# Kernel tuning notes

Hardware: AMD Instinct MI355X
Metric: run time of the kernel (lower is better)

The kernel has to match this reference:

```python
import jax, jax.numpy as jnp
import numpy as np

VOCAB = 50257
EMBED_DIM = 1024
FRONT_DIM = 2048  # int(embed_dim * front_embed_mul)
BATCH, SEQ = 4, 4096


def setup_inputs() -> dict:
    key = jax.random.key(0)
    k_idx, k_emb, k_w1, k_b1, k_w2, k_b2 = jax.random.split(key, 6)
    idxs = jax.random.randint(k_idx, (BATCH, SEQ), 0, VOCAB, dtype=jnp.int64)
    tok_embed = jax.random.normal(k_emb, (VOCAB, FRONT_DIM), dtype=jnp.float32)
    # torch nn.Linear weights are [out, in]
    W1 = jax.random.normal(k_w1, (EMBED_DIM, FRONT_DIM), dtype=jnp.float32) * (1.0 / np.sqrt(FRONT_DIM))
    b1 = jax.random.normal(k_b1, (EMBED_DIM,), dtype=jnp.float32) * 0.01
    W2 = jax.random.normal(k_w2, (EMBED_DIM, EMBED_DIM), dtype=jnp.float32) * (1.0 / np.sqrt(EMBED_DIM))
    b2 = jax.random.normal(k_b2, (EMBED_DIM,), dtype=jnp.float32) * 0.01
    return {"idxs": idxs, "tok_embed": tok_embed, "W1": W1, "b1": b1, "W2": W2, "b2": b2}


def reference(idxs, tok_embed, W1, b1, W2, b2):
    # Embedding gather: [B, S, front_dim]
    x = tok_embed[idxs]
    # integration1: Linear(front_dim -> embed_dim)
    x = jnp.einsum('bsf,ef->bse', x, W1) + b1
    # exact (erf-based) GELU, matching torch F.gelu default
    x = jax.nn.gelu(x, approximate=False)
    # integration2: Linear(embed_dim -> embed_dim)
    x = jnp.einsum('bse,oe->bso', x, W2) + b2
    return x
```

## Files before the change

kernel.cpp:

```cpp
#include <hip/hip_runtime.h>
#include <hip/hip_bf16.h>

typedef __attribute__((ext_vector_type(4))) float floatx4;
typedef __attribute__((ext_vector_type(8))) short short8;
typedef __attribute__((ext_vector_type(8))) unsigned short ushortx8;

#define K1 2048
#define N1 1024
#define K2 1024
#define N2 1024

__device__ __forceinline__ unsigned short f2bf(float f) {
  __hip_bfloat16 h = __float2bfloat16(f);
  return __builtin_bit_cast(unsigned short, h);
}

__device__ __forceinline__ void gload_lds16(const void* g, void* l) {
  __builtin_amdgcn_global_load_lds(
      (__attribute__((address_space(1))) void*)const_cast<void*>(g),
      (__attribute__((address_space(3))) void*)l, 16, 0, 0);
}

__global__ void cvt_bf16_kernel(const float* __restrict__ src,
                                unsigned short* __restrict__ dst, int n4) {
  int i = blockIdx.x * blockDim.x + threadIdx.x;
  if (i >= n4) return;
  float4 f = reinterpret_cast<const float4*>(src)[i];
  ushort4 o;
  o.x = f2bf(f.x); o.y = f2bf(f.y); o.z = f2bf(f.z); o.w = f2bf(f.w);
  reinterpret_cast<ushort4*>(dst)[i] = o;
}

__global__ __launch_bounds__(512, 2) void gemm1_fused_kernel(
    const int* __restrict__ idxs, const float* __restrict__ tok,
    const unsigned short* __restrict__ W1b, const float* __restrict__ b1,
    unsigned short* __restrict__ hout) {
  __shared__ unsigned short Asub[2][16384];
  __shared__ unsigned short Bsub[2][16384];
  const int t = threadIdx.x;
  const int p = blockIdx.x;
  const int bid = (p & 7) * 32 + (p >> 3);
  const int bm = bid >> 2, bn = bid & 3;
  const int brow0 = bm * 256, bcol0 = bn * 256;
  const int lane = t & 63, w = t >> 6;
  const int wm = w >> 2, wn = w & 3;
  const int fr = lane & 15, kg2 = lane >> 4;

  const int srow = t >> 3;
  const int cg = (t & 7) ^ (srow & 7);
  const float* aqf[4];
  const unsigned short* bq[4];
#pragma unroll
  for (int q = 0; q < 4; ++q) {
    const int ridx = idxs[brow0 + srow + 64 * q];
    aqf[q] = tok + (size_t)ridx * K1 + cg * 8;
    bq[q] = W1b + (size_t)(bcol0 + srow + 64 * q) * K1 + cg * 8;
  }
  const int t8 = t * 8;

  floatx4 acc[8][4] = {};
  constexpr int NT = K1 / 64;

  float4 av[4][2];
  auto loadA = [&](int k0) {
#pragma unroll
    for (int q = 0; q < 4; ++q) {
      av[q][0] = *reinterpret_cast<const float4*>(aqf[q] + k0);
      av[q][1] = *reinterpret_cast<const float4*>(aqf[q] + k0 + 4);
    }
  };
  auto writeA = [&](int d) {
#pragma unroll
    for (int q = 0; q < 4; ++q) {
      ushortx8 u;
      u[0] = f2bf(av[q][0].x); u[1] = f2bf(av[q][0].y);
      u[2] = f2bf(av[q][0].z); u[3] = f2bf(av[q][0].w);
      u[4] = f2bf(av[q][1].x); u[5] = f2bf(av[q][1].y);
      u[6] = f2bf(av[q][1].z); u[7] = f2bf(av[q][1].w);
      *reinterpret_cast<ushortx8*>(&Asub[d][t8 + q * 4096]) = u;
    }
  };
  auto issueB = [&](int d, int k0) {
#pragma unroll
    for (int q = 0; q < 4; ++q)
      gload_lds16(bq[q] + k0, &Bsub[d][t8 + q * 4096]);
  };
  auto computeKS = [&](int cur, int ks) {
    const int sl = ((ks * 4 + kg2) ^ (fr & 7)) * 8;
    short8 bf[4];
#pragma unroll
    for (int j = 0; j < 4; ++j)
      bf[j] = *(const short8*)&Bsub[cur][(wn * 64 + j * 16 + fr) * 64 + sl];
    __builtin_amdgcn_s_setprio(1);
#pragma unroll
    for (int i = 0; i < 8; ++i) {
      const short8 af = *(const short8*)&Asub[cur][(wm * 128 + i * 16 + fr) * 64 + sl];
#pragma unroll
      for (int j = 0; j < 4; ++j)
        acc[i][j] = __builtin_amdgcn_mfma_f32_16x16x32_bf16(af, bf[j], acc[i][j], 0, 0, 0);
    }
    __builtin_amdgcn_s_setprio(0);
  };

  loadA(0);
  issueB(0, 0);
  writeA(0);
  asm volatile("s_waitcnt vmcnt(0) lgkmcnt(0)\ns_barrier" ::: "memory");

#pragma unroll 1
  for (int tt = 0; tt < NT; ++tt) {
    const int cur = tt & 1;
    const int nbuf = cur ^ 1;
    const bool pf = (tt + 1 < NT);
    const int nk = (tt + 1) * 64;
    if (pf) {
      loadA(nk);
      issueB(nbuf, nk);
    }
    computeKS(cur, 0);
    if (pf) writeA(nbuf);
    computeKS(cur, 1);
    asm volatile("s_waitcnt vmcnt(0) lgkmcnt(0)\ns_barrier" ::: "memory");
  }

  const int er0 = brow0 + wm * 128 + kg2 * 4;
  const int ec0 = bcol0 + wn * 64 + fr;
#pragma unroll
  for (int j = 0; j < 4; ++j) {
    const float bv = b1[ec0 + j * 16];
#pragma unroll
    for (int i = 0; i < 8; ++i)
#pragma unroll
      for (int r = 0; r < 4; ++r) {
        float v = acc[i][j][r] + bv;
        v = 0.5f * v * (1.0f + erff(v * 0.70710678118654752f));
        hout[(size_t)(er0 + i * 16 + r) * N1 + (ec0 + j * 16)] = f2bf(v);
      }
  }
}

__global__ __launch_bounds__(512, 2) void gemm2_kernel(
    const unsigned short* __restrict__ A, const unsigned short* __restrict__ Bw,
    const float* __restrict__ bias, float* __restrict__ out) {
  __shared__ unsigned short Asub[2][16384];
  __shared__ unsigned short Bsub[2][16384];
  const int t = threadIdx.x;
  const int p = blockIdx.x;
  const int bid = (p & 7) * 32 + (p >> 3);
  const int bm = bid >> 2, bn = bid & 3;
  const int brow0 = bm * 256, bcol0 = bn * 256;
  const int lane = t & 63, w = t >> 6;
  const int wm = w >> 2, wn = w & 3;
  const int fr = lane & 15, kg2 = lane >> 4;

  const int srow = t >> 3;
  const int cg = (t & 7) ^ (srow & 7);
  const unsigned short* aq[4];
  const unsigned short* bq[4];
#pragma unroll
  for (int q = 0; q < 4; ++q) {
    aq[q] = A + (size_t)(brow0 + srow + 64 * q) * K2 + cg * 8;
    bq[q] = Bw + (size_t)(bcol0 + srow + 64 * q) * K2 + cg * 8;
  }
  const int t8 = t * 8;

  const int arow_sh = (wm * 128 + fr) * 64;
  const int brow_sh = (wn * 64 + fr) * 64;

  floatx4 acc[8][4] = {};
  constexpr int NT = K2 / 64;

  auto stage = [&](int d, int k0) {
#pragma unroll
    for (int q = 0; q < 4; ++q) {
      gload_lds16(aq[q] + k0, &Asub[d][t8 + q * 4096]);
      gload_lds16(bq[q] + k0, &Bsub[d][t8 + q * 4096]);
    }
  };
  auto compute = [&](int cur) {
#pragma unroll
    for (int ks = 0; ks < 2; ++ks) {
      const int sl = ((ks * 4 + kg2) ^ (fr & 7)) * 8;
      short8 bf[4];
#pragma unroll
      for (int j = 0; j < 4; ++j)
        bf[j] = *reinterpret_cast<const short8*>(&Bsub[cur][brow_sh + j * 1024 + sl]);
#pragma unroll
      for (int i = 0; i < 8; ++i) {
        const short8 af = *reinterpret_cast<const short8*>(&Asub[cur][arow_sh + i * 1024 + sl]);
#pragma unroll
        for (int j = 0; j < 4; ++j)
          acc[i][j] = __builtin_amdgcn_mfma_f32_16x16x32_bf16(af, bf[j], acc[i][j], 0, 0, 0);
      }
    }
  };

  stage(0, 0);
#pragma unroll 1
  for (int it = 0; it < NT - 1; ++it) {
    const int cur = it & 1;
    stage(cur ^ 1, (it + 1) * 64);
    asm volatile("s_waitcnt vmcnt(8)\ns_barrier" ::: "memory");
    compute(cur);
    asm volatile("s_waitcnt lgkmcnt(0)\ns_barrier" ::: "memory");
  }
  asm volatile("s_waitcnt vmcnt(0)\ns_barrier" ::: "memory");
  compute((NT - 1) & 1);

  const int er0 = brow0 + wm * 128 + kg2 * 4;
  const int ec0 = bcol0 + wn * 64 + fr;
#pragma unroll
  for (int j = 0; j < 4; ++j) {
    const float bv = bias[ec0 + j * 16];
#pragma unroll
    for (int i = 0; i < 8; ++i)
#pragma unroll
      for (int r = 0; r < 4; ++r)
        out[(size_t)(er0 + i * 16 + r) * N2 + (ec0 + j * 16)] = acc[i][j][r] + bv;
  }
}

extern "C" void kernel_launch(void* const* d_in, const int* in_sizes, int n_in,
                              void* d_out, int out_size, void* d_ws, size_t ws_size,
                              hipStream_t stream) {
  const int* idxs = (const int*)d_in[0];
  const float* tok = (const float*)d_in[1];
  const float* W1 = (const float*)d_in[2];
  const float* b1 = (const float*)d_in[3];
  const float* W2 = (const float*)d_in[4];
  const float* b2 = (const float*)d_in[5];
  float* out = (float*)d_out;

  unsigned short* W1b = (unsigned short*)d_ws;
  unsigned short* W2b = (unsigned short*)((char*)d_ws + (4u << 20));
  unsigned short* hbuf = (unsigned short*)((char*)d_ws + (6u << 20));

  cvt_bf16_kernel<<<2048, 256, 0, stream>>>(W1, W1b, 524288);
  cvt_bf16_kernel<<<1024, 256, 0, stream>>>(W2, W2b, 262144);
  gemm1_fused_kernel<<<256, 512, 0, stream>>>(idxs, tok, W1b, b1, hbuf);
  gemm2_kernel<<<256, 512, 0, stream>>>(hbuf, W2b, b2, out);
}
```

Before: 155.5 us.

## Stage GEMM epilogues through LDS for coalesced stores and merge weight conversions

Both GEMM epilogues now write their accumulator tiles into a per-wave swizzled LDS region (reusing the now-unified shared buffer), then read them back as 16-byte vectors so each row segment goes to global memory as one coalesced store. Before, each lane stored scattered 2-byte or 4-byte elements. The two weight-conversion launches are merged into a single kernel to save one launch. gemm2 also gains setprio around its MFMA loop. In exchange the epilogue adds LDS traffic and waitcnt/barrier overhead.

Result: faster. 140.9 us (-9.4%).

```diff
diff --git a/kernel.cpp b/kernel.cpp
--- a/kernel.cpp
+++ b/kernel.cpp
@@ -21,22 +21,32 @@
       (__attribute__((address_space(3))) void*)l, 16, 0, 0);
 }
 
-__global__ void cvt_bf16_kernel(const float* __restrict__ src,
-                                unsigned short* __restrict__ dst, int n4) {
+__global__ __launch_bounds__(256) void cvt2_kernel(
+    const float* __restrict__ W1, const float* __restrict__ W2,
+    unsigned short* __restrict__ W1b, unsigned short* __restrict__ W2b) {
   int i = blockIdx.x * blockDim.x + threadIdx.x;
-  if (i >= n4) return;
-  float4 f = reinterpret_cast<const float4*>(src)[i];
+  const float* src;
+  unsigned short* dst;
+  if (i < 524288) {
+    src = (const float*)&reinterpret_cast<const float4*>(W1)[i];
+    dst = (unsigned short*)&reinterpret_cast<ushort4*>(W1b)[i];
+  } else {
+    int k = i - 524288;
+    if (k >= 262144) return;
+    src = (const float*)&reinterpret_cast<const float4*>(W2)[k];
+    dst = (unsigned short*)&reinterpret_cast<ushort4*>(W2b)[k];
+  }
+  float4 f = *reinterpret_cast<const float4*>(src);
   ushort4 o;
   o.x = f2bf(f.x); o.y = f2bf(f.y); o.z = f2bf(f.z); o.w = f2bf(f.w);
-  reinterpret_cast<ushort4*>(dst)[i] = o;
+  *reinterpret_cast<ushort4*>(dst) = o;
 }
 
 __global__ __launch_bounds__(512, 2) void gemm1_fused_kernel(
     const int* __restrict__ idxs, const float* __restrict__ tok,
     const unsigned short* __restrict__ W1b, const float* __restrict__ b1,
     unsigned short* __restrict__ hout) {
-  __shared__ unsigned short Asub[2][16384];
-  __shared__ unsigned short Bsub[2][16384];
+  __shared__ unsigned short S[65536];
   const int t = threadIdx.x;
   const int p = blockIdx.x;
   const int bid = (p & 7) * 32 + (p >> 3);
@@ -77,24 +87,24 @@
       u[2] = f2bf(av[q][0].z); u[3] = f2bf(av[q][0].w);
       u[4] = f2bf(av[q][1].x); u[5] = f2bf(av[q][1].y);
       u[6] = f2bf(av[q][1].z); u[7] = f2bf(av[q][1].w);
-      *reinterpret_cast<ushortx8*>(&Asub[d][t8 + q * 4096]) = u;
+      *reinterpret_cast<ushortx8*>(&S[d * 16384 + t8 + q * 4096]) = u;
     }
   };
   auto issueB = [&](int d, int k0) {
 #pragma unroll
     for (int q = 0; q < 4; ++q)
-      gload_lds16(bq[q] + k0, &Bsub[d][t8 + q * 4096]);
+      gload_lds16(bq[q] + k0, &S[32768 + d * 16384 + t8 + q * 4096]);
   };
   auto computeKS = [&](int cur, int ks) {
     const int sl = ((ks * 4 + kg2) ^ (fr & 7)) * 8;
     short8 bf[4];
 #pragma unroll
     for (int j = 0; j < 4; ++j)
-      bf[j] = *(const short8*)&Bsub[cur][(wn * 64 + j * 16 + fr) * 64 + sl];
+      bf[j] = *(const short8*)&S[32768 + cur * 16384 + (wn * 64 + j * 16 + fr) * 64 + sl];
     __builtin_amdgcn_s_setprio(1);
 #pragma unroll
     for (int i = 0; i < 8; ++i) {
-      const short8 af = *(const short8*)&Asub[cur][(wm * 128 + i * 16 + fr) * 64 + sl];
+      const short8 af = *(const short8*)&S[cur * 16384 + (wm * 128 + i * 16 + fr) * 64 + sl];
 #pragma unroll
       for (int j = 0; j < 4; ++j)
         acc[i][j] = __builtin_amdgcn_mfma_f32_16x16x32_bf16(af, bf[j], acc[i][j], 0, 0, 0);
@@ -123,27 +133,38 @@
     asm volatile("s_waitcnt vmcnt(0) lgkmcnt(0)\ns_barrier" ::: "memory");
   }
 
-  const int er0 = brow0 + wm * 128 + kg2 * 4;
   const int ec0 = bcol0 + wn * 64 + fr;
-#pragma unroll
-  for (int j = 0; j < 4; ++j) {
-    const float bv = b1[ec0 + j * 16];
-#pragma unroll
-    for (int i = 0; i < 8; ++i)
+  float bv[4];
+#pragma unroll
+  for (int j = 0; j < 4; ++j) bv[j] = b1[ec0 + j * 16];
+  unsigned short* Wl = S + w * 8192;
+#pragma unroll
+  for (int i = 0; i < 8; ++i)
+#pragma unroll
+    for (int j = 0; j < 4; ++j)
 #pragma unroll
       for (int r = 0; r < 4; ++r) {
-        float v = acc[i][j][r] + bv;
+        float v = acc[i][j][r] + bv[j];
         v = 0.5f * v * (1.0f + erff(v * 0.70710678118654752f));
-        hout[(size_t)(er0 + i * 16 + r) * N1 + (ec0 + j * 16)] = f2bf(v);
+        const int row = i * 16 + kg2 * 4 + r;
+        const int col = (j * 16 + fr) ^ (kg2 << 3);
+        Wl[row * 64 + col] = f2bf(v);
       }
+  asm volatile("s_waitcnt lgkmcnt(0)" ::: "memory");
+#pragma unroll
+  for (int pass = 0; pass < 16; ++pass) {
+    const int wr = pass * 8 + (lane >> 3);
+    const int ch = (lane & 7) ^ ((wr >> 2) & 3);
+    const short8 v8 = *(const short8*)&Wl[wr * 64 + ch * 8];
+    *reinterpret_cast<short8*>(
+        &hout[(size_t)(brow0 + wm * 128 + wr) * N1 + bcol0 + wn * 64 + (lane & 7) * 8]) = v8;
   }
 }
 
 __global__ __launch_bounds__(512, 2) void gemm2_kernel(
     const unsigned short* __restrict__ A, const unsigned short* __restrict__ Bw,
     const float* __restrict__ bias, float* __restrict__ out) {
-  __shared__ unsigned short Asub[2][16384];
-  __shared__ unsigned short Bsub[2][16384];
+  __shared__ unsigned short S[65536];
   const int t = threadIdx.x;
   const int p = blockIdx.x;
   const int bid = (p & 7) * 32 + (p >> 3);
@@ -164,17 +185,14 @@
   }
   const int t8 = t * 8;
 
-  const int arow_sh = (wm * 128 + fr) * 64;
-  const int brow_sh = (wn * 64 + fr) * 64;
-
   floatx4 acc[8][4] = {};
   constexpr int NT = K2 / 64;
 
   auto stage = [&](int d, int k0) {
 #pragma unroll
     for (int q = 0; q < 4; ++q) {
-      gload_lds16(aq[q] + k0, &Asub[d][t8 + q * 4096]);
-      gload_lds16(bq[q] + k0, &Bsub[d][t8 + q * 4096]);
+      gload_lds16(aq[q] + k0, &S[d * 16384 + t8 + q * 4096]);
+      gload_lds16(bq[q] + k0, &S[32768 + d * 16384 + t8 + q * 4096]);
     }
   };
   auto compute = [&](int cur) {
@@ -184,14 +202,16 @@
       short8 bf[4];
 #pragma unroll
       for (int j = 0; j < 4; ++j)
-        bf[j] = *reinterpret_cast<const short8*>(&Bsub[cur][brow_sh + j * 1024 + sl]);
+        bf[j] = *(const short8*)&S[32768 + cur * 16384 + (wn * 64 + j * 16 + fr) * 64 + sl];
+      __builtin_amdgcn_s_setprio(1);
 #pragma unroll
       for (int i = 0; i < 8; ++i) {
-        const short8 af = *reinterpret_cast<const short8*>(&Asub[cur][arow_sh + i * 1024 + sl]);
+        const short8 af = *(const short8*)&S[cur * 16384 + (wm * 128 + i * 16 + fr) * 64 + sl];
 #pragma unroll
         for (int j = 0; j < 4; ++j)
           acc[i][j] = __builtin_amdgcn_mfma_f32_16x16x32_bf16(af, bf[j], acc[i][j], 0, 0, 0);
       }
+      __builtin_amdgcn_s_setprio(0);
     }
   };
 
@@ -206,17 +226,37 @@
   }
   asm volatile("s_waitcnt vmcnt(0)\ns_barrier" ::: "memory");
   compute((NT - 1) & 1);
-
-  const int er0 = brow0 + wm * 128 + kg2 * 4;
+  asm volatile("s_waitcnt lgkmcnt(0)\ns_barrier" ::: "memory");
+
   const int ec0 = bcol0 + wn * 64 + fr;
-#pragma unroll
-  for (int j = 0; j < 4; ++j) {
-    const float bv = bias[ec0 + j * 16];
-#pragma unroll
-    for (int i = 0; i < 8; ++i)
-#pragma unroll
-      for (int r = 0; r < 4; ++r)
-        out[(size_t)(er0 + i * 16 + r) * N2 + (ec0 + j * 16)] = acc[i][j][r] + bv;
+  float bv[4];
+#pragma unroll
+  for (int j = 0; j < 4; ++j) bv[j] = bias[ec0 + j * 16];
+  float* Wf = reinterpret_cast<float*>(S) + w * 4096;
+#pragma unroll
+  for (int ih = 0; ih < 2; ++ih) {
+#pragma unroll
+    for (int i4 = 0; i4 < 4; ++i4)
+#pragma unroll
+      for (int j = 0; j < 4; ++j)
+#pragma unroll
+        for (int r = 0; r < 4; ++r) {
+          const int row = i4 * 16 + kg2 * 4 + r;
+          const int col = (j * 16 + fr) ^ (kg2 << 2);
+          Wf[row * 64 + col] = acc[ih * 4 + i4][j][r] + bv[j];
+        }
+    asm volatile("s_waitcnt lgkmcnt(0)" ::: "memory");
+#pragma unroll
+    for (int pass = 0; pass < 16; ++pass) {
+      const int wr = pass * 4 + (lane >> 4);
+      const int ch = (lane & 15) ^ ((wr >> 2) & 3);
+      const floatx4 v4 = *(const floatx4*)&Wf[wr * 64 + ch * 4];
+      *reinterpret_cast<floatx4*>(
+          &out[(size_t)(brow0 + wm * 128 + ih * 64 + wr) * N2 + bcol0 + wn * 64 +
+               (lane & 15) * 4]) = v4;
+    }
+    if (ih == 0)
+      asm volatile("s_waitcnt lgkmcnt(0)" ::: "memory");
   }
 }
 
@@ -235,8 +275,7 @@
   unsigned short* W2b = (unsigned short*)((char*)d_ws + (4u << 20));
   unsigned short* hbuf = (unsigned short*)((char*)d_ws + (6u << 20));
 
-  cvt_bf16_kernel<<<2048, 256, 0, stream>>>(W1, W1b, 524288);
-  cvt_bf16_kernel<<<1024, 256, 0, stream>>>(W2, W2b, 262144);
+  cvt2_kernel<<<3072, 256, 0, stream>>>(W1, W2, W1b, W2b);
   gemm1_fused_kernel<<<256, 512, 0, stream>>>(idxs, tok, W1b, b1, hbuf);
   gemm2_kernel<<<256, 512, 0, stream>>>(hbuf, W2b, b2, out);
 }
```
